# Kernel optimization log

Hardware: AMD Instinct MI355X
Metric: run time of the kernel (lower is better)

Reference implementation:

```python
import jax, jax.numpy as jnp
import numpy as np

E = 1024
H = 16
F = 4096
EPS = 1e-5


def layer_norm(x, gamma, beta):
    mu = jnp.mean(x, axis=-1, keepdims=True)
    var = jnp.var(x, axis=-1, keepdims=True)
    return (x - mu) * jax.lax.rsqrt(var + EPS) * gamma + beta


def setup_inputs() -> dict:
    key = jax.random.key(0)
    ks = jax.random.split(key, 12)
    s = lambda d: 1.0 / np.sqrt(d)
    x = jax.random.normal(ks[0], (2, 2048, E), dtype=jnp.float32)
    Wq = jax.random.uniform(ks[1], (E, E), minval=-s(E), maxval=s(E))
    bq = jnp.zeros((E,), jnp.float32)
    Wk = jax.random.uniform(ks[2], (E, E), minval=-s(E), maxval=s(E))
    bk = jnp.zeros((E,), jnp.float32)
    Wv = jax.random.uniform(ks[3], (E, E), minval=-s(E), maxval=s(E))
    bv = jnp.zeros((E,), jnp.float32)
    Wo = jax.random.uniform(ks[4], (E, E), minval=-s(E), maxval=s(E))
    bo = jnp.zeros((E,), jnp.float32)
    g1 = jnp.ones((E,), jnp.float32)
    b1 = jnp.zeros((E,), jnp.float32)
    W1 = jax.random.uniform(ks[5], (E, F), minval=-s(E), maxval=s(E))
    bf1 = jnp.zeros((F,), jnp.float32)
    W2 = jax.random.uniform(ks[6], (F, E), minval=-s(F), maxval=s(F))
    bf2 = jnp.zeros((E,), jnp.float32)
    g2 = jnp.ones((E,), jnp.float32)
    b2 = jnp.zeros((E,), jnp.float32)
    return dict(x=x, Wq=Wq, bq=bq, Wk=Wk, bk=bk, Wv=Wv, bv=bv, Wo=Wo, bo=bo,
                g1=g1, b1=b1, W1=W1, bf1=bf1, W2=W2, bf2=bf2, g2=g2, b2=b2)


def reference(x, Wq, bq, Wk, bk, Wv, bv, Wo, bo, g1, b1, W1, bf1, W2, bf2, g2, b2):
    B, L, _ = x.shape
    Dh = E // H
    q = (x @ Wq + bq).reshape(B, L, H, Dh).transpose(0, 2, 1, 3)  # b h l d
    k = (x @ Wk + bk).reshape(B, L, H, Dh).transpose(0, 2, 1, 3)  # computed but unused (faithful to source)
    v = (x @ Wv + bv).reshape(B, L, H, Dh).transpose(0, 2, 1, 3)
    # NOTE: source computes scores as Q @ V^T (not K), scaled, then softmax
    scores = jnp.einsum('bhqd,bhkd->bhqk', q, v) / jnp.sqrt(jnp.float32(Dh))
    att = jax.nn.softmax(scores, axis=-1)
    ctx = jnp.einsum('bhqk,bhkd->bhqd', att, v)
    ctx = ctx.transpose(0, 2, 1, 3).reshape(B, L, E)
    att_out = ctx @ Wo + bo
    post_att = layer_norm(x + att_out, g1, b1)
    ff = jax.nn.relu(post_att @ W1 + bf1) @ W2 + bf2
    return layer_norm(post_att + ff, g2, b2)
```

## Files before the change

### kernel.cpp

```cpp
#include <hip/hip_runtime.h>
#include <stdint.h>

typedef unsigned short u16;
typedef __attribute__((ext_vector_type(8))) short short8;
typedef __attribute__((ext_vector_type(4))) float f32x4;
typedef __attribute__((ext_vector_type(4))) unsigned short u16x4;

#define TOKENS 4096
#define E_DIM 1024
#define F_DIM 4096
#define SEQ 2048
#define NH 16
#define DH 64

__device__ __forceinline__ u16 f2b(float f) {
  union { float f; unsigned u; } v; v.f = f;
  unsigned r = v.u + 0x7fffu + ((v.u >> 16) & 1u);
  return (u16)(r >> 16);
}

__device__ __forceinline__ void gl2lds16(const u16* g, u16* l) {
  __builtin_amdgcn_global_load_lds(
      (const __attribute__((address_space(1))) unsigned int*)(size_t)(g),
      (__attribute__((address_space(3))) unsigned int*)(unsigned int)(size_t)(l),
      16, 0, 0);
}


__global__ __launch_bounds__(256)
void transpose_w3(const float* __restrict__ W0, const float* __restrict__ W1s,
                  const float* __restrict__ W2s, u16* __restrict__ T0,
                  u16* __restrict__ T1, u16* __restrict__ T2) {
  __shared__ float tile[32][33];
  const float* W = (blockIdx.z == 0) ? W0 : (blockIdx.z == 1) ? W1s : W2s;
  u16* Wt = (blockIdx.z == 0) ? T0 : (blockIdx.z == 1) ? T1 : T2;
  const int kb = blockIdx.x * 32, nb = blockIdx.y * 32;
  const int tx = threadIdx.x & 31, ty = threadIdx.x >> 5;
#pragma unroll
  for (int i = 0; i < 32; i += 8)
    tile[ty + i][tx] = W[(size_t)(kb + ty + i) * 1024 + nb + tx];
  __syncthreads();
#pragma unroll
  for (int i = 0; i < 32; i += 8)
    Wt[(size_t)(nb + ty + i) * 1024 + kb + tx] = f2b(tile[tx][ty + i]);
}

__global__ __launch_bounds__(256)
void transpose_w(const float* __restrict__ W, u16* __restrict__ Wt, int K, int N) {
  __shared__ float tile[32][33];
  const int kb = blockIdx.x * 32, nb = blockIdx.y * 32;
  const int tx = threadIdx.x & 31, ty = threadIdx.x >> 5;
#pragma unroll
  for (int i = 0; i < 32; i += 8)
    tile[ty + i][tx] = W[(size_t)(kb + ty + i) * N + nb + tx];
  __syncthreads();
#pragma unroll
  for (int i = 0; i < 32; i += 8)
    Wt[(size_t)(nb + ty + i) * K + kb + tx] = f2b(tile[tx][ty + i]);
}

__global__ __launch_bounds__(256)
void f32_to_bf16(const float* __restrict__ in, u16* __restrict__ out) {
  const int i = blockIdx.x * 256 + threadIdx.x;
  f32x4 f = ((const f32x4*)in)[i];
  u16x4 u;
#pragma unroll
  for (int j = 0; j < 4; j++) u[j] = f2b(f[j]);
  ((u16x4*)out)[i] = u;
}

__global__ __launch_bounds__(256)
void transpose_v(const u16* __restrict__ vsrc, u16* __restrict__ vt) {
  __shared__ u16 tile[64][66];
  const int kb = blockIdx.x * 64;
  const int bh = blockIdx.y;
  const int b = bh >> 4, h = bh & 15;
  {
    const int d = threadIdx.x & 63, r = threadIdx.x >> 6;
#pragma unroll
    for (int i = 0; i < 64; i += 4)
      tile[r + i][d] = vsrc[(size_t)(b * SEQ + kb + r + i) * E_DIM + h * DH + d];
  }
  __syncthreads();
  {
    const int pos = threadIdx.x & 63;
    const int srck = ((pos >> 5) << 5) | (((pos >> 2) & 1) << 4) |
                     (((pos >> 3) & 3) << 2) | (pos & 3);
#pragma unroll
    for (int j = 0; j < 64; j += 4) {
      const int d = (threadIdx.x >> 6) + j;
      vt[(size_t)(bh * DH + d) * SEQ + kb + pos] = tile[srck][d];
    }
  }
}

template <int RELU, int OUTBF>
__global__ __launch_bounds__(512)
void gemm256(const u16* __restrict__ A, const u16* __restrict__ Bt,
             const float* __restrict__ bias, void* __restrict__ Cout,
             int N, int K) {
  __shared__ __align__(16) u16 lds[3][2][8192];
  const int tid = threadIdx.x;
  const int lane = tid & 63, wave = tid >> 6;
  const int wm = wave >> 2, wn = wave & 3;
  const int l15 = lane & 15, g = lane >> 4;

  const int bid = blockIdx.x;
  const int xcd = bid & 7, idx = bid >> 3;
  const int mT = (xcd >> 2) * 8 + (idx >> 2);
  const int nT = (xcd & 3) * 4 + (idx & 3);
  const int mBlk = mT * 256, nBlk = nT * 256;

  const u16* Ab = A + (size_t)mBlk * K;
  const u16* Bb = Bt + (size_t)nBlk * K;

  const int srow = lane >> 2;
  const int scolx = ((lane & 3) ^ ((lane >> 3) & 3)) * 8;
  const u16* sa0 = Ab + (size_t)(wave * 16 + srow) * K + scolx;
  const u16* sa1 = Ab + (size_t)((8 + wave) * 16 + srow) * K + scolx;
  const u16* sb0 = Bb + (size_t)(wave * 16 + srow) * K + scolx;
  const u16* sb1 = Bb + (size_t)((8 + wave) * 16 + srow) * K + scolx;

  const int fo = l15 * 32 + ((g ^ ((l15 >> 1) & 3)) << 3);

  f32x4 acc[8][4] = {};

  const int NT = K >> 5;

#define STAGE_A(buf, t)                                             \
  {                                                                 \
    gl2lds16(sa0 + (size_t)(t) * 32, &lds[buf][0][wave * 512 + lane * 8]);       \
    gl2lds16(sa1 + (size_t)(t) * 32, &lds[buf][0][(8 + wave) * 512 + lane * 8]); \
  }
#define STAGE_B(buf, t)                                             \
  {                                                                 \
    gl2lds16(sb0 + (size_t)(t) * 32, &lds[buf][1][wave * 512 + lane * 8]);       \
    gl2lds16(sb1 + (size_t)(t) * 32, &lds[buf][1][(8 + wave) * 512 + lane * 8]); \
  }

  STAGE_A(0, 0) STAGE_B(0, 0)
  STAGE_A(1, 1) STAGE_B(1, 1)
  asm volatile("s_waitcnt vmcnt(4)" ::: "memory");
  asm volatile("s_barrier" ::: "memory");

  int buf = 0, sbuf = 2;
  for (int t = 0; t < NT; ++t) {
    const u16* As_ = &lds[buf][0][wm * (8 * 512)];
    const u16* Bs_ = &lds[buf][1][wn * (4 * 512)];

    short8 af[4], bfr[4];
#pragma unroll
    for (int i = 0; i < 4; i++)
      af[i] = *(const short8*)(As_ + i * 512 + fo);
#pragma unroll
    for (int i = 0; i < 4; i++)
      bfr[i] = *(const short8*)(Bs_ + i * 512 + fo);
    if (t + 2 < NT) STAGE_A(sbuf, t + 2)
    asm volatile("s_barrier" ::: "memory");
    asm volatile("s_waitcnt lgkmcnt(0)" ::: "memory");
    __builtin_amdgcn_sched_barrier(0);
    __builtin_amdgcn_s_setprio(1);
#pragma unroll
    for (int mg = 0; mg < 4; mg++)
#pragma unroll
      for (int ng = 0; ng < 4; ng++)
        acc[mg][ng] = __builtin_amdgcn_mfma_f32_16x16x32_bf16(af[mg], bfr[ng],
                                                              acc[mg][ng], 0, 0, 0);
    __builtin_amdgcn_s_setprio(0);
    asm volatile("s_barrier" ::: "memory");

#pragma unroll
    for (int i = 0; i < 4; i++)
      af[i] = *(const short8*)(As_ + (4 + i) * 512 + fo);
    if (t + 2 < NT) STAGE_B(sbuf, t + 2)
    asm volatile("s_barrier" ::: "memory");
    asm volatile("s_waitcnt lgkmcnt(0)" ::: "memory");
    __builtin_amdgcn_sched_barrier(0);
    __builtin_amdgcn_s_setprio(1);
#pragma unroll
    for (int mg = 0; mg < 4; mg++)
#pragma unroll
      for (int ng = 0; ng < 4; ng++)
        acc[4 + mg][ng] = __builtin_amdgcn_mfma_f32_16x16x32_bf16(af[mg], bfr[ng],
                                                                  acc[4 + mg][ng], 0, 0, 0);
    __builtin_amdgcn_s_setprio(0);
    if (t + 2 < NT) asm volatile("s_waitcnt vmcnt(4)" ::: "memory");
    else            asm volatile("s_waitcnt vmcnt(0)" ::: "memory");
    asm volatile("s_barrier" ::: "memory");

    buf = (buf == 2) ? 0 : buf + 1;
    sbuf = (sbuf == 2) ? 0 : sbuf + 1;
  }
#undef STAGE_A
#undef STAGE_B

  const int row0 = mBlk + wm * 128 + g * 4;
  const int col0 = nBlk + wn * 64 + l15;
#pragma unroll
  for (int ng = 0; ng < 4; ng++) {
    const int c = col0 + ng * 16;
    const float bv = bias[c];
#pragma unroll
    for (int mg = 0; mg < 8; mg++) {
#pragma unroll
      for (int r = 0; r < 4; r++) {
        float v = acc[mg][ng][r] + bv;
        if (RELU) v = fmaxf(v, 0.f);
        const size_t o = (size_t)(row0 + mg * 16 + r) * N + c;
        if (OUTBF) ((u16*)Cout)[o] = f2b(v);
        else       ((float*)Cout)[o] = v;
      }
    }
  }
}

__global__ __launch_bounds__(512)
void gemm_wide_sk(const u16* __restrict__ A, const u16* __restrict__ Bt,
                  const float* __restrict__ bias, float* __restrict__ Cout,
                  int N, int K) {
  __shared__ __align__(16) u16 lds[3][12288];
  const int tid = threadIdx.x;
  const int lane = tid & 63, wave = tid >> 6;
  const int wm = wave >> 1, wn = wave & 1;
  const int l15 = lane & 15, g = lane >> 4;

  const int bid = blockIdx.x;
  const int xcd = bid & 7, idx = bid >> 3;
  const int kz = xcd & 1;
  const int nT = ((xcd >> 1) & 1) * 4 + (idx & 3);
  const int mT = (xcd >> 2) * 8 + (idx >> 2);
  const int mBlk = mT * 256, nBlk = nT * 128;
  const int Kh = K >> 1;

  const u16* Ab = A + (size_t)mBlk * K + (size_t)kz * Kh;
  const u16* Bb = Bt + (size_t)nBlk * K + (size_t)kz * Kh;

  const int srow = lane >> 2;
  const int scolx = ((lane & 3) ^ ((lane >> 3) & 3)) * 8;
  const u16* sa0 = Ab + (size_t)(wave * 16 + srow) * K + scolx;
  const u16* sa1 = Ab + (size_t)((8 + wave) * 16 + srow) * K + scolx;
  const u16* sb0 = Bb + (size_t)(wave * 16 + srow) * K + scolx;

  const int fo = l15 * 32 + ((g ^ ((l15 >> 1) & 3)) << 3);

  f32x4 acc[4][4] = {};
  const int NT = Kh >> 5;

#define WSTAGE(buf, t)                                                         \
  {                                                                            \
    gl2lds16(sa0 + (size_t)(t) * 32, &lds[buf][wave * 512 + lane * 8]);        \
    gl2lds16(sa1 + (size_t)(t) * 32, &lds[buf][(8 + wave) * 512 + lane * 8]);  \
    gl2lds16(sb0 + (size_t)(t) * 32, &lds[buf][8192 + wave * 512 + lane * 8]); \
  }

  WSTAGE(0, 0)
  WSTAGE(1, 1)
  asm volatile("s_waitcnt vmcnt(3)" ::: "memory");
  asm volatile("s_barrier" ::: "memory");

  int buf = 0, sbuf = 2;
  for (int t = 0; t < NT; ++t) {
    const u16* As_ = &lds[buf][wm * (4 * 512)];
    const u16* Bs_ = &lds[buf][8192 + wn * (4 * 512)];
    short8 af[4], bfr[4];
#pragma unroll
    for (int i = 0; i < 4; i++)
      af[i] = *(const short8*)(As_ + i * 512 + fo);
#pragma unroll
    for (int i = 0; i < 4; i++)
      bfr[i] = *(const short8*)(Bs_ + i * 512 + fo);
    if (t + 2 < NT) WSTAGE(sbuf, t + 2)
    asm volatile("s_waitcnt lgkmcnt(0)" ::: "memory");
    __builtin_amdgcn_sched_barrier(0);
    __builtin_amdgcn_s_setprio(1);
#pragma unroll
    for (int mi = 0; mi < 4; mi++)
#pragma unroll
      for (int ni = 0; ni < 4; ni++)
        acc[mi][ni] = __builtin_amdgcn_mfma_f32_16x16x32_bf16(af[mi], bfr[ni],
                                                              acc[mi][ni], 0, 0, 0);
    __builtin_amdgcn_s_setprio(0);
    if (t + 2 < NT) asm volatile("s_waitcnt vmcnt(3)" ::: "memory");
    else            asm volatile("s_waitcnt vmcnt(0)" ::: "memory");
    asm volatile("s_barrier" ::: "memory");
    buf = (buf == 2) ? 0 : buf + 1;
    sbuf = (sbuf == 2) ? 0 : sbuf + 1;
  }
#undef WSTAGE

  float* out = Cout + (size_t)kz * TOKENS * N;
  const int row0 = mBlk + wm * 64 + g * 4;
  const int col0 = nBlk + wn * 64 + l15;
#pragma unroll
  for (int ni = 0; ni < 4; ni++) {
    const int c = col0 + ni * 16;
    const float bv = (kz == 0) ? bias[c] : 0.f;
#pragma unroll
    for (int mi = 0; mi < 4; mi++) {
#pragma unroll
      for (int r = 0; r < 4; r++)
        out[(size_t)(row0 + mi * 16 + r) * N + c] = acc[mi][ni][r] + bv;
    }
  }
}

__global__ __launch_bounds__(512)
void gemm_qv(const u16* __restrict__ A, const u16* __restrict__ Bqv,
             const float* __restrict__ bq, const float* __restrict__ bv,
             u16* __restrict__ qout, u16* __restrict__ vout, int K) {
  __shared__ __align__(16) u16 lds[3][12288];
  const int tid = threadIdx.x;
  const int lane = tid & 63, wave = tid >> 6;
  const int wm = wave >> 1, wn = wave & 1;
  const int l15 = lane & 15, g = lane >> 4;

  const int bid = blockIdx.x;
  const int xcd = bid & 7, idx = bid >> 3;
  const int mT = (xcd >> 1) * 4 + (idx >> 3);
  const int nT = (xcd & 1) * 8 + (idx & 7);
  const int mBlk = mT * 256, nBlkG = nT * 128;

  const int isQ = nT < 8;
  const int ncol = isQ ? nBlkG : nBlkG - 1024;
  const float* bias = isQ ? bq : bv;
  u16* out = isQ ? qout : vout;
  const float oscale = isQ ? 0.125f * 1.44269504088896f : 1.0f;

  const u16* Ab = A + (size_t)mBlk * K;
  const u16* Bb = Bqv + (size_t)nBlkG * K;

  const int srow = lane >> 2;
  const int scolx = ((lane & 3) ^ ((lane >> 3) & 3)) * 8;
  const u16* sa0 = Ab + (size_t)(wave * 16 + srow) * K + scolx;
  const u16* sa1 = Ab + (size_t)((8 + wave) * 16 + srow) * K + scolx;
  const u16* sb0 = Bb + (size_t)(wave * 16 + srow) * K + scolx;

  const int fo = l15 * 32 + ((g ^ ((l15 >> 1) & 3)) << 3);

  f32x4 acc[4][4] = {};
  const int NT = K >> 5;

#define QSTAGE(buf, t)                                                         \
  {                                                                            \
    gl2lds16(sa0 + (size_t)(t) * 32, &lds[buf][wave * 512 + lane * 8]);        \
    gl2lds16(sa1 + (size_t)(t) * 32, &lds[buf][(8 + wave) * 512 + lane * 8]);  \
    gl2lds16(sb0 + (size_t)(t) * 32, &lds[buf][8192 + wave * 512 + lane * 8]); \
  }

  QSTAGE(0, 0)
  QSTAGE(1, 1)
  asm volatile("s_waitcnt vmcnt(3)" ::: "memory");
  asm volatile("s_barrier" ::: "memory");

  int buf = 0, sbuf = 2;
  for (int t = 0; t < NT; ++t) {
    const u16* As_ = &lds[buf][wm * (4 * 512)];
    const u16* Bs_ = &lds[buf][8192 + wn * (4 * 512)];
    short8 af[4], bfr[4];
#pragma unroll
    for (int i = 0; i < 4; i++)
      af[i] = *(const short8*)(As_ + i * 512 + fo);
#pragma unroll
    for (int i = 0; i < 4; i++)
      bfr[i] = *(const short8*)(Bs_ + i * 512 + fo);
    if (t + 2 < NT) QSTAGE(sbuf, t + 2)
    asm volatile("s_waitcnt lgkmcnt(0)" ::: "memory");
    __builtin_amdgcn_sched_barrier(0);
    __builtin_amdgcn_s_setprio(1);
#pragma unroll
    for (int mi = 0; mi < 4; mi++)
#pragma unroll
      for (int ni = 0; ni < 4; ni++)
        acc[mi][ni] = __builtin_amdgcn_mfma_f32_16x16x32_bf16(af[mi], bfr[ni],
                                                              acc[mi][ni], 0, 0, 0);
    __builtin_amdgcn_s_setprio(0);
    if (t + 2 < NT) asm volatile("s_waitcnt vmcnt(3)" ::: "memory");
    else            asm volatile("s_waitcnt vmcnt(0)" ::: "memory");
    asm volatile("s_barrier" ::: "memory");
    buf = (buf == 2) ? 0 : buf + 1;
    sbuf = (sbuf == 2) ? 0 : sbuf + 1;
  }
#undef QSTAGE

  const int row0 = mBlk + wm * 64 + g * 4;
  const int col0 = ncol + wn * 64 + l15;
#pragma unroll
  for (int ni = 0; ni < 4; ni++) {
    const int c = col0 + ni * 16;
    const float bv_ = bias[c];
#pragma unroll
    for (int mi = 0; mi < 4; mi++) {
#pragma unroll
      for (int r = 0; r < 4; r++) {
        float v = (acc[mi][ni][r] + bv_) * oscale;
        out[(size_t)(row0 + mi * 16 + r) * E_DIM + c] = f2b(v);
      }
    }
  }
}

__global__ __launch_bounds__(256)
void attn_kernel(const u16* __restrict__ qb, const u16* __restrict__ vb,
                 const u16* __restrict__ vtb, u16* __restrict__ ctxb) {
  __shared__ __align__(16) u16 Vs[2][4096];
  __shared__ __align__(16) u16 Vts[2][4096];
  const int tid = threadIdx.x;
  const int lane = tid & 63;
  const int wave = tid >> 6;
  const int l15 = lane & 15;
  const int g = lane >> 4;
  const int l7 = l15 & 7;
  const int qblk = blockIdx.x;
  const int bh = blockIdx.y;
  const int b = bh >> 4;
  const int h = bh & 15;
  const int qrow = qblk * 64 + wave * 16;

  short8 aq0, aq1;
  {
    const u16* qp = qb + ((size_t)(b * SEQ + qrow + l15)) * E_DIM + h * DH + g * 8;
    aq0 = *(const short8*)(qp);
    aq1 = *(const short8*)(qp + 32);
  }

  f32x4 o[4] = {};
  float lsum = 0.f;

  const u16* qk0b0 = Vs[0] + l15 * 64 + ((g ^ l7) * 8);
  const u16* qk1b0 = Vs[0] + l15 * 64 + (((4 + g) ^ l7) * 8);
  const u16* bv0b0 = Vts[0] + l15 * 64 + ((g ^ l7) * 8);
  const u16* bv1b0 = Vts[0] + l15 * 64 + (((4 + g) ^ l7) * 8);

  const int srow = tid >> 3;
  const int sch = tid & 7;
  const int r0 = srow, r1 = 32 + srow;
  const u16* pv0 = vb + ((size_t)(b * SEQ) + r0) * E_DIM + h * DH + ((sch ^ (r0 & 7)) * 8);
  const u16* pv1 = vb + ((size_t)(b * SEQ) + r1) * E_DIM + h * DH + ((sch ^ (r1 & 7)) * 8);
  const u16* pt0 = vtb + ((size_t)bh * DH + r0) * SEQ + ((sch ^ (r0 & 7)) * 8);
  const u16* pt1 = vtb + ((size_t)bh * DH + r1) * SEQ + ((sch ^ (r1 & 7)) * 8);

#define STAGE(buf)                                      \
  {                                                     \
    gl2lds16(pv0, Vs[buf] + tid * 8);                   \
    gl2lds16(pv1, Vs[buf] + 2048 + tid * 8);            \
    gl2lds16(pt0, Vts[buf] + tid * 8);                  \
    gl2lds16(pt1, Vts[buf] + 2048 + tid * 8);           \
    pv0 += 64 * E_DIM; pv1 += 64 * E_DIM;               \
    pt0 += 64; pt1 += 64;                               \
  }

#define COMPUTE(QK0, QK1, BV0, BV1)                                           \
  {                                                                           \
    f32x4 s[4];                                                               \
    _Pragma("unroll") for (int nt = 0; nt < 4; nt++) {                        \
      short8 b0 = *(const short8*)((QK0) + nt * 1024);                        \
      short8 b1 = *(const short8*)((QK1) + nt * 1024);                        \
      f32x4 z = {};                                                           \
      z = __builtin_amdgcn_mfma_f32_16x16x32_bf16(b0, aq0, z, 0, 0, 0);       \
      z = __builtin_amdgcn_mfma_f32_16x16x32_bf16(b1, aq1, z, 0, 0, 0);       \
      s[nt] = z;                                                              \
    }                                                                         \
    union { unsigned w[4]; short8 v; } pa0, pa1;                              \
    {                                                                         \
      unsigned pu[4][4];                                                      \
      float ls = 0.f;                                                         \
      _Pragma("unroll") for (int nt = 0; nt < 4; nt++) {                      \
        _Pragma("unroll") for (int r = 0; r < 4; r++) {                       \
          union { float f; unsigned u; } e;                                   \
          e.f = __builtin_amdgcn_exp2f(s[nt][r]);                             \
          pu[nt][r] = e.u;                                                    \
          union { unsigned u; float f; } t; t.u = e.u & 0xffff0000u;          \
          ls += t.f;                                                          \
        }                                                                     \
      }                                                                       \
      lsum += ls;                                                             \
      pa0.w[0] = __builtin_amdgcn_perm(pu[0][1], pu[0][0], 0x07060302u);      \
      pa0.w[1] = __builtin_amdgcn_perm(pu[0][3], pu[0][2], 0x07060302u);      \
      pa0.w[2] = __builtin_amdgcn_perm(pu[1][1], pu[1][0], 0x07060302u);      \
      pa0.w[3] = __builtin_amdgcn_perm(pu[1][3], pu[1][2], 0x07060302u);      \
      pa1.w[0] = __builtin_amdgcn_perm(pu[2][1], pu[2][0], 0x07060302u);      \
      pa1.w[1] = __builtin_amdgcn_perm(pu[2][3], pu[2][2], 0x07060302u);      \
      pa1.w[2] = __builtin_amdgcn_perm(pu[3][1], pu[3][0], 0x07060302u);      \
      pa1.w[3] = __builtin_amdgcn_perm(pu[3][3], pu[3][2], 0x07060302u);      \
    }                                                                         \
    _Pragma("unroll") for (int dt = 0; dt < 4; dt++) {                        \
      short8 bvv = *(const short8*)((BV0) + dt * 1024);                       \
      o[dt] = __builtin_amdgcn_mfma_f32_16x16x32_bf16(pa0.v, bvv, o[dt], 0, 0, 0); \
    }                                                                         \
    _Pragma("unroll") for (int dt = 0; dt < 4; dt++) {                        \
      short8 bvv = *(const short8*)((BV1) + dt * 1024);                       \
      o[dt] = __builtin_amdgcn_mfma_f32_16x16x32_bf16(pa1.v, bvv, o[dt], 0, 0, 0); \
    }                                                                         \
  }

#define HALF(CB, EN)                                                          \
  {                                                                           \
    asm volatile("s_barrier" ::: "memory");                                   \
    if (EN) {                                                                 \
      STAGE(CB ^ 1)                                                           \
      asm volatile("s_waitcnt vmcnt(4)" ::: "memory");                        \
    } else {                                                                  \
      asm volatile("s_waitcnt vmcnt(0)" ::: "memory");                        \
    }                                                                         \
    asm volatile("s_barrier" ::: "memory");                                   \
    if (CB == 0) { COMPUTE(qk0b0, qk1b0, bv0b0, bv1b0) }                      \
    else { COMPUTE(qk0b0 + 4096, qk1b0 + 4096, bv0b0 + 4096, bv1b0 + 4096) }  \
  }

  STAGE(0)
#pragma unroll 1
  for (int it = 0; it < 15; ++it) {
    HALF(0, 1)
    HALF(1, 1)
  }
  HALF(0, 1)
  HALF(1, 0)

#undef HALF
#undef COMPUTE
#undef STAGE

  lsum += __shfl_xor(lsum, 16);
  lsum += __shfl_xor(lsum, 32);
#pragma unroll
  for (int r = 0; r < 4; r++) {
    const float inv = 1.0f / __shfl(lsum, g * 4 + r);
    size_t base = ((size_t)(b * SEQ + qrow + g * 4 + r)) * E_DIM + h * DH;
#pragma unroll
    for (int dt = 0; dt < 4; dt++)
      ctxb[base + dt * 16 + l15] = f2b(o[dt][r] * inv);
  }
}

__global__ __launch_bounds__(256)
void add_ln3(const float* __restrict__ X, const float* __restrict__ Y0,
             const float* __restrict__ Y1,
             const float* __restrict__ gam, const float* __restrict__ bet,
             float* __restrict__ out32, u16* __restrict__ out16) {
  const int row = blockIdx.x;
  const int tid = threadIdx.x;
  const size_t base = (size_t)row * E_DIM;
  const int c4 = tid * 4;
  f32x4 x = *(const f32x4*)(X + base + c4);
  f32x4 y0 = *(const f32x4*)(Y0 + base + c4);
  f32x4 y1 = *(const f32x4*)(Y1 + base + c4);
  f32x4 v;
  float s = 0.f, sq = 0.f;
#pragma unroll
  for (int i = 0; i < 4; i++) {
    float t = x[i] + y0[i] + y1[i];
    v[i] = t; s += t; sq += t * t;
  }
#pragma unroll
  for (int off = 32; off; off >>= 1) {
    s += __shfl_xor(s, off);
    sq += __shfl_xor(sq, off);
  }
  __shared__ float sh[8];
  const int wave = tid >> 6, lane = tid & 63;
  if (lane == 0) { sh[wave] = s; sh[4 + wave] = sq; }
  __syncthreads();
  s = sh[0] + sh[1] + sh[2] + sh[3];
  sq = sh[4] + sh[5] + sh[6] + sh[7];
  const float mean = s * (1.f / 1024.f);
  const float var = sq * (1.f / 1024.f) - mean * mean;
  const float rstd = rsqrtf(var + 1e-5f);
  f32x4 gm = *(const f32x4*)(gam + c4);
  f32x4 bt = *(const f32x4*)(bet + c4);
  f32x4 y;
  u16x4 yb;
#pragma unroll
  for (int i = 0; i < 4; i++) {
    y[i] = (v[i] - mean) * rstd * gm[i] + bt[i];
    yb[i] = f2b(y[i]);
  }
  *(f32x4*)(out32 + base + c4) = y;
  if (out16) *(u16x4*)(out16 + base + c4) = yb;
}

extern "C" void kernel_launch(void* const* d_in, const int* in_sizes, int n_in,
                              void* d_out, int out_size, void* d_ws, size_t ws_size,
                              hipStream_t stream) {
  const float* x   = (const float*)d_in[0];
  const float* Wq  = (const float*)d_in[1];
  const float* bq  = (const float*)d_in[2];
  const float* Wv  = (const float*)d_in[5];
  const float* bv  = (const float*)d_in[6];
  const float* Wo  = (const float*)d_in[7];
  const float* bo  = (const float*)d_in[8];
  const float* g1  = (const float*)d_in[9];
  const float* b1  = (const float*)d_in[10];
  const float* W1  = (const float*)d_in[11];
  const float* bf1 = (const float*)d_in[12];
  const float* W2  = (const float*)d_in[13];
  const float* bf2 = (const float*)d_in[14];
  const float* g2  = (const float*)d_in[15];
  const float* b2  = (const float*)d_in[16];

  char* w = (char*)d_ws;
  const size_t MB = 1024ull * 1024ull;
  u16*   xb   = (u16*)(w + 0);
  u16*   h1   = (u16*)(w + 8 * MB);
  u16*   qb   = (u16*)(w + 8 * MB);
  u16*   vb   = (u16*)(w + 16 * MB);
  u16*   vtb  = (u16*)(w + 24 * MB);
  u16*   ctxb = (u16*)(w + 32 * MB);
  float* att0 = (float*)(w + 40 * MB);
  float* ff0  = (float*)(w + 40 * MB);
  float* pa   = (float*)(w + 72 * MB);
  u16*   pab  = (u16*)(w + 88 * MB);
  u16*   WqT  = (u16*)(w + 96 * MB);
  u16*   WvT  = (u16*)(w + 98 * MB);
  u16*   WoT  = (u16*)(w + 100 * MB);
  u16*   W1T  = (u16*)(w + 102 * MB);
  u16*   W2T  = (u16*)(w + 110 * MB);

  transpose_w3<<<dim3(32, 32, 3), 256, 0, stream>>>(Wq, Wv, Wo, WqT, WvT, WoT);
  transpose_w<<<dim3(32, 128), 256, 0, stream>>>(W1, W1T, 1024, 4096);
  transpose_w<<<dim3(128, 32), 256, 0, stream>>>(W2, W2T, 4096, 1024);
  f32_to_bf16<<<TOKENS * E_DIM / 4 / 256, 256, 0, stream>>>(x, xb);

  gemm_qv<<<dim3(256), 512, 0, stream>>>(xb, WqT, bq, bv, qb, vb, 1024);
  transpose_v<<<dim3(32, 32), 256, 0, stream>>>(vb, vtb);
  attn_kernel<<<dim3(32, 32), 256, 0, stream>>>(qb, vb, vtb, ctxb);
  gemm_wide_sk<<<dim3(256), 512, 0, stream>>>(ctxb, WoT, bo, att0, 1024, 1024);
  add_ln3<<<TOKENS, 256, 0, stream>>>(x, att0, att0 + (size_t)TOKENS * 1024, g1, b1, pa, pab);
  gemm256<1, 1><<<dim3(256), 512, 0, stream>>>(pab, W1T, bf1, h1, 4096, 1024);
  gemm_wide_sk<<<dim3(256), 512, 0, stream>>>(h1, W2T, bf2, ff0, 1024, 4096);
  add_ln3<<<TOKENS, 256, 0, stream>>>(pa, ff0, ff0 + (size_t)TOKENS * 1024, g2, b2, (float*)d_out, (u16*)nullptr);
}
```

Before: 341.2 us.

## Process two 16-row query tiles per wave in attention, halve block threads

The attention kernel now runs 2 waves per block instead of 4, and each wave handles 32 query rows (two 16-row MFMA tiles). Each LDS fragment of V and V^T is loaded once and used for both tiles, so LDS read traffic per MFMA is halved. Staging is redistributed so 128 threads each issue 8 global-to-LDS loads, and the wait count is raised to match. The cost is higher register pressure from doubled accumulators and softmax temporaries, and fewer waves per block to hide latency.

Measured after the change: 337.3 us. Within noise of the previous version (-1.1%).

```diff
diff --git a/kernel.cpp b/kernel.cpp
--- a/kernel.cpp
+++ b/kernel.cpp
@@ -399,7 +399,7 @@
   }
 }
 
-__global__ __launch_bounds__(256)
+__global__ __launch_bounds__(128)
 void attn_kernel(const u16* __restrict__ qb, const u16* __restrict__ vb,
                  const u16* __restrict__ vtb, u16* __restrict__ ctxb) {
   __shared__ __align__(16) u16 Vs[2][4096];
@@ -414,17 +414,20 @@
   const int bh = blockIdx.y;
   const int b = bh >> 4;
   const int h = bh & 15;
-  const int qrow = qblk * 64 + wave * 16;
-
-  short8 aq0, aq1;
+  const int qrow = qblk * 64 + wave * 32;
+
+  short8 aq00, aq01, aq10, aq11;
   {
-    const u16* qp = qb + ((size_t)(b * SEQ + qrow + l15)) * E_DIM + h * DH + g * 8;
-    aq0 = *(const short8*)(qp);
-    aq1 = *(const short8*)(qp + 32);
-  }
-
-  f32x4 o[4] = {};
-  float lsum = 0.f;
+    const u16* qp0 = qb + ((size_t)(b * SEQ + qrow + l15)) * E_DIM + h * DH + g * 8;
+    const u16* qp1 = qb + ((size_t)(b * SEQ + qrow + 16 + l15)) * E_DIM + h * DH + g * 8;
+    aq00 = *(const short8*)(qp0);
+    aq01 = *(const short8*)(qp0 + 32);
+    aq10 = *(const short8*)(qp1);
+    aq11 = *(const short8*)(qp1 + 32);
+  }
+
+  f32x4 o0[4] = {}, o1[4] = {};
+  float lsum0 = 0.f, lsum1 = 0.f;
 
   const u16* qk0b0 = Vs[0] + l15 * 64 + ((g ^ l7) * 8);
   const u16* qk1b0 = Vs[0] + l15 * 64 + (((4 + g) ^ l7) * 8);
@@ -433,63 +436,74 @@
 
   const int srow = tid >> 3;
   const int sch = tid & 7;
-  const int r0 = srow, r1 = 32 + srow;
-  const u16* pv0 = vb + ((size_t)(b * SEQ) + r0) * E_DIM + h * DH + ((sch ^ (r0 & 7)) * 8);
-  const u16* pv1 = vb + ((size_t)(b * SEQ) + r1) * E_DIM + h * DH + ((sch ^ (r1 & 7)) * 8);
-  const u16* pt0 = vtb + ((size_t)bh * DH + r0) * SEQ + ((sch ^ (r0 & 7)) * 8);
-  const u16* pt1 = vtb + ((size_t)bh * DH + r1) * SEQ + ((sch ^ (r1 & 7)) * 8);
+  const int sx = (sch ^ (srow & 7)) * 8;
+  const u16* pv[4];
+  const u16* pt[4];
+#pragma unroll
+  for (int j = 0; j < 4; j++) {
+    pv[j] = vb + ((size_t)(b * SEQ) + j * 16 + srow) * E_DIM + h * DH + sx;
+    pt[j] = vtb + ((size_t)bh * DH + j * 16 + srow) * SEQ + sx;
+  }
 
 #define STAGE(buf)                                      \
   {                                                     \
-    gl2lds16(pv0, Vs[buf] + tid * 8);                   \
-    gl2lds16(pv1, Vs[buf] + 2048 + tid * 8);            \
-    gl2lds16(pt0, Vts[buf] + tid * 8);                  \
-    gl2lds16(pt1, Vts[buf] + 2048 + tid * 8);           \
-    pv0 += 64 * E_DIM; pv1 += 64 * E_DIM;               \
-    pt0 += 64; pt1 += 64;                               \
+    _Pragma("unroll") for (int j = 0; j < 4; j++) {     \
+      gl2lds16(pv[j], Vs[buf] + j * 1024 + tid * 8);    \
+      gl2lds16(pt[j], Vts[buf] + j * 1024 + tid * 8);   \
+      pv[j] += 64 * E_DIM;                              \
+      pt[j] += 64;                                      \
+    }                                                   \
+  }
+
+#define SOFTMAX(S, PA0, PA1, LS)                                              \
+  {                                                                           \
+    unsigned pu[4][4];                                                        \
+    float ls = 0.f;                                                           \
+    _Pragma("unroll") for (int nt = 0; nt < 4; nt++) {                        \
+      _Pragma("unroll") for (int r = 0; r < 4; r++) {                         \
+        union { float f; unsigned u; } e;                                     \
+        e.f = __builtin_amdgcn_exp2f(S[nt][r]);                               \
+        pu[nt][r] = e.u;                                                      \
+        union { unsigned u; float f; } t; t.u = e.u & 0xffff0000u;            \
+        ls += t.f;                                                            \
+      }                                                                       \
+    }                                                                         \
+    LS += ls;                                                                 \
+    PA0.w[0] = __builtin_amdgcn_perm(pu[0][1], pu[0][0], 0x07060302u);        \
+    PA0.w[1] = __builtin_amdgcn_perm(pu[0][3], pu[0][2], 0x07060302u);        \
+    PA0.w[2] = __builtin_amdgcn_perm(pu[1][1], pu[1][0], 0x07060302u);        \
+    PA0.w[3] = __builtin_amdgcn_perm(pu[1][3], pu[1][2], 0x07060302u);        \
+    PA1.w[0] = __builtin_amdgcn_perm(pu[2][1], pu[2][0], 0x07060302u);        \
+    PA1.w[1] = __builtin_amdgcn_perm(pu[2][3], pu[2][2], 0x07060302u);        \
+    PA1.w[2] = __builtin_amdgcn_perm(pu[3][1], pu[3][0], 0x07060302u);        \
+    PA1.w[3] = __builtin_amdgcn_perm(pu[3][3], pu[3][2], 0x07060302u);        \
   }
 
 #define COMPUTE(QK0, QK1, BV0, BV1)                                           \
   {                                                                           \
-    f32x4 s[4];                                                               \
+    f32x4 s0[4], s1[4];                                                       \
     _Pragma("unroll") for (int nt = 0; nt < 4; nt++) {                        \
       short8 b0 = *(const short8*)((QK0) + nt * 1024);                        \
       short8 b1 = *(const short8*)((QK1) + nt * 1024);                        \
-      f32x4 z = {};                                                           \
-      z = __builtin_amdgcn_mfma_f32_16x16x32_bf16(b0, aq0, z, 0, 0, 0);       \
-      z = __builtin_amdgcn_mfma_f32_16x16x32_bf16(b1, aq1, z, 0, 0, 0);       \
-      s[nt] = z;                                                              \
+      f32x4 z0 = {}, z1 = {};                                                 \
+      z0 = __builtin_amdgcn_mfma_f32_16x16x32_bf16(b0, aq00, z0, 0, 0, 0);    \
+      z0 = __builtin_amdgcn_mfma_f32_16x16x32_bf16(b1, aq01, z0, 0, 0, 0);    \
+      z1 = __builtin_amdgcn_mfma_f32_16x16x32_bf16(b0, aq10, z1, 0, 0, 0);    \
+      z1 = __builtin_amdgcn_mfma_f32_16x16x32_bf16(b1, aq11, z1, 0, 0, 0);    \
+      s0[nt] = z0; s1[nt] = z1;                                               \
     }                                                                         \
-    union { unsigned w[4]; short8 v; } pa0, pa1;                              \
-    {                                                                         \
-      unsigned pu[4][4];                                                      \
-      float ls = 0.f;                                                         \
-      _Pragma("unroll") for (int nt = 0; nt < 4; nt++) {                      \
-        _Pragma("unroll") for (int r = 0; r < 4; r++) {                       \
-          union { float f; unsigned u; } e;                                   \
-          e.f = __builtin_amdgcn_exp2f(s[nt][r]);                             \
-          pu[nt][r] = e.u;                                                    \
-          union { unsigned u; float f; } t; t.u = e.u & 0xffff0000u;          \
-          ls += t.f;                                                          \
-        }                                                                     \
-      }                                                                       \
-      lsum += ls;                                                             \
-      pa0.w[0] = __builtin_amdgcn_perm(pu[0][1], pu[0][0], 0x07060302u);      \
-      pa0.w[1] = __builtin_amdgcn_perm(pu[0][3], pu[0][2], 0x07060302u);      \
-      pa0.w[2] = __builtin_amdgcn_perm(pu[1][1], pu[1][0], 0x07060302u);      \
-      pa0.w[3] = __builtin_amdgcn_perm(pu[1][3], pu[1][2], 0x07060302u);      \
-      pa1.w[0] = __builtin_amdgcn_perm(pu[2][1], pu[2][0], 0x07060302u);      \
-      pa1.w[1] = __builtin_amdgcn_perm(pu[2][3], pu[2][2], 0x07060302u);      \
-      pa1.w[2] = __builtin_amdgcn_perm(pu[3][1], pu[3][0], 0x07060302u);      \
-      pa1.w[3] = __builtin_amdgcn_perm(pu[3][3], pu[3][2], 0x07060302u);      \
-    }                                                                         \
+    union { unsigned w[4]; short8 v; } paA0, paB0, paA1, paB1;                \
+    SOFTMAX(s0, paA0, paB0, lsum0)                                            \
+    SOFTMAX(s1, paA1, paB1, lsum1)                                            \
     _Pragma("unroll") for (int dt = 0; dt < 4; dt++) {                        \
       short8 bvv = *(const short8*)((BV0) + dt * 1024);                       \
-      o[dt] = __builtin_amdgcn_mfma_f32_16x16x32_bf16(pa0.v, bvv, o[dt], 0, 0, 0); \
+      o0[dt] = __builtin_amdgcn_mfma_f32_16x16x32_bf16(paA0.v, bvv, o0[dt], 0, 0, 0); \
+      o1[dt] = __builtin_amdgcn_mfma_f32_16x16x32_bf16(paA1.v, bvv, o1[dt], 0, 0, 0); \
     }                                                                         \
     _Pragma("unroll") for (int dt = 0; dt < 4; dt++) {                        \
       short8 bvv = *(const short8*)((BV1) + dt * 1024);                       \
-      o[dt] = __builtin_amdgcn_mfma_f32_16x16x32_bf16(pa1.v, bvv, o[dt], 0, 0, 0); \
+      o0[dt] = __builtin_amdgcn_mfma_f32_16x16x32_bf16(paB0.v, bvv, o0[dt], 0, 0, 0); \
+      o1[dt] = __builtin_amdgcn_mfma_f32_16x16x32_bf16(paB1.v, bvv, o1[dt], 0, 0, 0); \
     }                                                                         \
   }
 
@@ -498,7 +512,7 @@
     asm volatile("s_barrier" ::: "memory");                                   \
     if (EN) {                                                                 \
       STAGE(CB ^ 1)                                                           \
-      asm volatile("s_waitcnt vmcnt(4)" ::: "memory");                        \
+      asm volatile("s_waitcnt vmcnt(8)" ::: "memory");                        \
     } else {                                                                  \
       asm volatile("s_waitcnt vmcnt(0)" ::: "memory");                        \
     }                                                                         \
@@ -518,17 +532,24 @@
 
 #undef HALF
 #undef COMPUTE
+#undef SOFTMAX
 #undef STAGE
 
-  lsum += __shfl_xor(lsum, 16);
-  lsum += __shfl_xor(lsum, 32);
+  lsum0 += __shfl_xor(lsum0, 16);
+  lsum0 += __shfl_xor(lsum0, 32);
+  lsum1 += __shfl_xor(lsum1, 16);
+  lsum1 += __shfl_xor(lsum1, 32);
 #pragma unroll
   for (int r = 0; r < 4; r++) {
-    const float inv = 1.0f / __shfl(lsum, g * 4 + r);
-    size_t base = ((size_t)(b * SEQ + qrow + g * 4 + r)) * E_DIM + h * DH;
-#pragma unroll
-    for (int dt = 0; dt < 4; dt++)
-      ctxb[base + dt * 16 + l15] = f2b(o[dt][r] * inv);
+    const float inv0 = 1.0f / __shfl(lsum0, g * 4 + r);
+    const float inv1 = 1.0f / __shfl(lsum1, g * 4 + r);
+    size_t base0 = ((size_t)(b * SEQ + qrow + g * 4 + r)) * E_DIM + h * DH;
+    size_t base1 = ((size_t)(b * SEQ + qrow + 16 + g * 4 + r)) * E_DIM + h * DH;
+#pragma unroll
+    for (int dt = 0; dt < 4; dt++) {
+      ctxb[base0 + dt * 16 + l15] = f2b(o0[dt][r] * inv0);
+      ctxb[base1 + dt * 16 + l15] = f2b(o1[dt][r] * inv1);
+    }
   }
 }
 
@@ -622,7 +643,7 @@
 
   gemm_qv<<<dim3(256), 512, 0, stream>>>(xb, WqT, bq, bv, qb, vb, 1024);
   transpose_v<<<dim3(32, 32), 256, 0, stream>>>(vb, vtb);
-  attn_kernel<<<dim3(32, 32), 256, 0, stream>>>(qb, vb, vtb, ctxb);
+  attn_kernel<<<dim3(32, 32), 128, 0, stream>>>(qb, vb, vtb, ctxb);
   gemm_wide_sk<<<dim3(256), 512, 0, stream>>>(ctxb, WoT, bo, att0, 1024, 1024);
   add_ln3<<<TOKENS, 256, 0, stream>>>(x, att0, att0 + (size_t)TOKENS * 1024, g1, b1, pa, pab);
   gemm256<1, 1><<<dim3(256), 512, 0, stream>>>(pab, W1T, bf1, h1, 4096, 1024);
```
